# Kernel optimization log

Hardware: AMD Instinct MI355X
Metric: run time of the kernel (lower is better)

## Reference

```python
import jax, jax.numpy as jnp
import numpy as np

B = 2048      # graphs per side
NPG = 40      # nodes per graph
N = B * NPG   # 81920 total nodes
E = 4 * N     # 327680 directed edges
IN_DIM = 74
H = 256
ADD = 8
GCR_LAYERS = 5
MLP1, MLP2 = 1024, 512


def setup_inputs() -> dict:
    key = jax.random.key(0)
    ks = jax.random.split(key, 24)
    n2g = jnp.repeat(jnp.arange(B, dtype=jnp.int32), NPG)
    s = 0.05
    d = {
        'cat_src': jax.random.randint(ks[0], (E,), 0, N, dtype=jnp.int32),
        'cat_dst': jax.random.randint(ks[1], (E,), 0, N, dtype=jnp.int32),
        'cat_n2g': n2g,
        'cat_x': jax.random.normal(ks[2], (N, IN_DIM), jnp.float32),
        'an_src': jax.random.randint(ks[3], (E,), 0, N, dtype=jnp.int32),
        'an_dst': jax.random.randint(ks[4], (E,), 0, N, dtype=jnp.int32),
        'an_n2g': n2g,
        'an_x': jax.random.normal(ks[5], (N, IN_DIM), jnp.float32),
        'add_features': jax.random.normal(ks[6], (B, ADD), jnp.float32),
        # shared GNN params (same module processes cation and anion)
        'W0': jax.random.normal(ks[7], (IN_DIM, H), jnp.float32) * s,
        'b0': jnp.zeros((H,), jnp.float32),
        'gcrW': jax.random.normal(ks[8], (GCR_LAYERS, 2, H, H), jnp.float32) * s,
        'gcrb': jnp.zeros((GCR_LAYERS, 2, H), jnp.float32),
        # MLP head: (2H + ADD) -> 1024 -> 512 -> 1
        'mW1': jax.random.normal(ks[9], (2 * H + ADD, MLP1), jnp.float32) * s,
        'mb1': jnp.zeros((MLP1,), jnp.float32),
        'mW2': jax.random.normal(ks[10], (MLP1, MLP2), jnp.float32) * s,
        'mb2': jnp.zeros((MLP2,), jnp.float32),
        'mW3': jax.random.normal(ks[11], (MLP2, 1), jnp.float32) * s,
        'mb3': jnp.zeros((1,), jnp.float32),
    }
    return d


def _graph_conv(src, dst, x, W, b):
    # DGL GraphConv, norm='both': out = D_in^{-1/2} A^T D_out^{-1/2} x W + b
    ones = jnp.ones(src.shape[0], x.dtype)
    deg_out = jnp.clip(jax.ops.segment_sum(ones, src, num_segments=N), 1.0)
    deg_in = jnp.clip(jax.ops.segment_sum(ones, dst, num_segments=N), 1.0)
    h = x * jax.lax.rsqrt(deg_out)[:, None]
    agg = jax.ops.segment_sum(h[src], dst, num_segments=N)  # [N, d]
    return (agg * jax.lax.rsqrt(deg_in)[:, None]) @ W + b


def _feat_extract(src, dst, n2g, x, W0, b0, gcrW, gcrb):
    h = _graph_conv(src, dst, x, W0, b0)  # no activation after first conv
    for i in range(GCR_LAYERS):
        o1 = _graph_conv(src, dst, h, gcrW[i, 0], gcrb[i, 0])
        o2 = _graph_conv(src, dst, jax.nn.relu(o1), gcrW[i, 1], gcrb[i, 1])
        h = jax.nn.relu(o2)  # res_connection = 0 -> plain replace
    # dgl.sum_nodes readout per graph
    return jax.ops.segment_sum(h, n2g, num_segments=B)  # [B, H]


def _leaky(x):
    return jnp.where(x > 0, x, 0.01 * x)  # nn.LeakyReLU default slope


def reference(cat_src, cat_dst, cat_n2g, cat_x, an_src, an_dst, an_n2g, an_x,
              add_features, W0, b0, gcrW, gcrb, mW1, mb1, mW2, mb2, mW3, mb3):
    cat_feat = _feat_extract(cat_src, cat_dst, cat_n2g, cat_x, W0, b0, gcrW, gcrb)
    an_feat = _feat_extract(an_src, an_dst, an_n2g, an_x, W0, b0, gcrW, gcrb)
    z = jnp.concatenate([cat_feat, an_feat, add_features], axis=1)  # [B, 2H+ADD]
    h = _leaky(z @ mW1 + mb1)
    h = _leaky(h @ mW2 + mb2)
    out = h @ mW3 + mb3  # [B, 1]
    return out.squeeze(-1)
```

## Files before the change

### kernel.cpp

```cpp
#include <hip/hip_runtime.h>


#define NN 81920
#define NN2 163840
#define NE 327680
#define NE2 655360
#define NB 2048
#define NB2 4096
#define H 256
#define INDIM 74
#define KPAD 128
#define ZK 576
#define DEGCAP 32
#define CPITCH 132

typedef unsigned short u16;
typedef __attribute__((ext_vector_type(8))) short short8;
typedef __attribute__((ext_vector_type(4))) float f32x4;

__device__ inline u16 f2b(float f) {
    unsigned u = __builtin_bit_cast(unsigned, f);
    u += 0x7fffu + ((u >> 16) & 1u);
    return (u16)(u >> 16);
}
__device__ inline float b2f(u16 b) {
    unsigned u = ((unsigned)b) << 16;
    return __builtin_bit_cast(float, u);
}
__device__ inline float blo(unsigned u) { return __builtin_bit_cast(float, u << 16); }
__device__ inline float bhi(unsigned u) { return __builtin_bit_cast(float, u & 0xffff0000u); }

__global__ void fill_kernel(const int* __restrict__ cs, const int* __restrict__ cd,
                            const int* __restrict__ as_, const int* __restrict__ ad,
                            int* __restrict__ dego, int* __restrict__ cnti,
                            int* __restrict__ bucket) {
    int e = blockIdx.x * 256 + threadIdx.x;
    if (e < NE2) {
        int s, d;
        if (e < NE) { s = cs[e]; d = cd[e]; }
        else        { s = as_[e - NE] + NN; d = ad[e - NE] + NN; }
        atomicAdd(&dego[s], 1);
        int p = atomicAdd(&cnti[d], 1);
        if (p < DEGCAP) bucket[(size_t)p * NN2 + d] = s;
    }
}

__global__ void rsqrt_kernel(const int* __restrict__ dego, const int* __restrict__ cnti,
                             float* __restrict__ rso, float* __restrict__ rsi) {
    int i = blockIdx.x * 256 + threadIdx.x;
    if (i < NN2) {
        rso[i] = rsqrtf((float)(dego[i] > 1 ? dego[i] : 1));
        rsi[i] = rsqrtf((float)(cnti[i] > 1 ? cnti[i] : 1));
    }
}

__global__ __launch_bounds__(256) void prescale_x_kernel(
        const float* __restrict__ cx, const float* __restrict__ ax,
        const float* __restrict__ rso, u16* __restrict__ xbp) {
    int t = threadIdx.x;
    int node = blockIdx.x * 4 + (t >> 6);
    int lane = t & 63;
    const float* x = (node < NN) ? (cx + (size_t)node * INDIM)
                                 : (ax + (size_t)(node - NN) * INDIM);
    float w = rso[node];
    int f0 = lane * 2, f1 = f0 + 1;
    u16 a = (f0 < INDIM) ? f2b(x[f0] * w) : (u16)0;
    u16 b = (f1 < INDIM) ? f2b(x[f1] * w) : (u16)0;
    ((unsigned*)xbp)[(size_t)node * 64 + lane] = a | ((unsigned)b << 16);
}

__global__ __launch_bounds__(256) void gather_x_kernel(
        const u16* __restrict__ xbp, const int* __restrict__ bucket,
        const int* __restrict__ cnti, const float* __restrict__ rsi,
        u16* __restrict__ out) {
    int node = blockIdx.x * 16 + (threadIdx.x >> 4);
    int fc = (threadIdx.x & 15) * 8;
    int deg = cnti[node]; if (deg > DEGCAP) deg = DEGCAP;
    const int* bk = bucket + node;
    float acc[8] = {};
    for (int base = 0; base < deg; base += 4) {
        int i0 = bk[(size_t)base * NN2];
        int i1 = (base + 1 < deg) ? bk[(size_t)(base + 1) * NN2] : i0;
        int i2 = (base + 2 < deg) ? bk[(size_t)(base + 2) * NN2] : i0;
        int i3 = (base + 3 < deg) ? bk[(size_t)(base + 3) * NN2] : i0;
        float m1 = (base + 1 < deg) ? 1.f : 0.f;
        float m2 = (base + 2 < deg) ? 1.f : 0.f;
        float m3 = (base + 3 < deg) ? 1.f : 0.f;
        uint4 v0 = *(const uint4*)(xbp + (size_t)i0 * KPAD + fc);
        uint4 v1 = *(const uint4*)(xbp + (size_t)i1 * KPAD + fc);
        uint4 v2 = *(const uint4*)(xbp + (size_t)i2 * KPAD + fc);
        uint4 v3 = *(const uint4*)(xbp + (size_t)i3 * KPAD + fc);
        acc[0] += blo(v0.x) + m1 * blo(v1.x) + m2 * blo(v2.x) + m3 * blo(v3.x);
        acc[1] += bhi(v0.x) + m1 * bhi(v1.x) + m2 * bhi(v2.x) + m3 * bhi(v3.x);
        acc[2] += blo(v0.y) + m1 * blo(v1.y) + m2 * blo(v2.y) + m3 * blo(v3.y);
        acc[3] += bhi(v0.y) + m1 * bhi(v1.y) + m2 * bhi(v2.y) + m3 * bhi(v3.y);
        acc[4] += blo(v0.z) + m1 * blo(v1.z) + m2 * blo(v2.z) + m3 * blo(v3.z);
        acc[5] += bhi(v0.z) + m1 * bhi(v1.z) + m2 * bhi(v2.z) + m3 * bhi(v3.z);
        acc[6] += blo(v0.w) + m1 * blo(v1.w) + m2 * blo(v2.w) + m3 * blo(v3.w);
        acc[7] += bhi(v0.w) + m1 * bhi(v1.w) + m2 * bhi(v2.w) + m3 * bhi(v3.w);
    }
    float ri = rsi[node];
    u16 o[8];
#pragma unroll
    for (int i = 0; i < 8; ++i) o[i] = f2b(acc[i] * ri);
    uint4 ov;
    ov.x = o[0] | ((unsigned)o[1] << 16);
    ov.y = o[2] | ((unsigned)o[3] << 16);
    ov.z = o[4] | ((unsigned)o[5] << 16);
    ov.w = o[6] | ((unsigned)o[7] << 16);
    *(uint4*)(out + (size_t)node * KPAD + fc) = ov;
}

__global__ __launch_bounds__(256) void gather_h_kernel(
        const u16* __restrict__ h, const int* __restrict__ bucket,
        const int* __restrict__ cnti, const float* __restrict__ rso,
        const float* __restrict__ rsi, u16* __restrict__ out) {
    int node = blockIdx.x * 8 + (threadIdx.x >> 5);
    int fc = (threadIdx.x & 31) * 8;
    int deg = cnti[node]; if (deg > DEGCAP) deg = DEGCAP;
    const int* bk = bucket + node;
    float acc[8] = {};
    for (int base = 0; base < deg; base += 4) {
        int i0 = bk[(size_t)base * NN2];
        int i1 = (base + 1 < deg) ? bk[(size_t)(base + 1) * NN2] : i0;
        int i2 = (base + 2 < deg) ? bk[(size_t)(base + 2) * NN2] : i0;
        int i3 = (base + 3 < deg) ? bk[(size_t)(base + 3) * NN2] : i0;
        float w0 = rso[i0];
        float w1 = (base + 1 < deg) ? rso[i1] : 0.f;
        float w2 = (base + 2 < deg) ? rso[i2] : 0.f;
        float w3 = (base + 3 < deg) ? rso[i3] : 0.f;
        uint4 v0 = *(const uint4*)(h + (size_t)i0 * H + fc);
        uint4 v1 = *(const uint4*)(h + (size_t)i1 * H + fc);
        uint4 v2 = *(const uint4*)(h + (size_t)i2 * H + fc);
        uint4 v3 = *(const uint4*)(h + (size_t)i3 * H + fc);
        acc[0] += blo(v0.x) * w0 + blo(v1.x) * w1 + blo(v2.x) * w2 + blo(v3.x) * w3;
        acc[1] += bhi(v0.x) * w0 + bhi(v1.x) * w1 + bhi(v2.x) * w2 + bhi(v3.x) * w3;
        acc[2] += blo(v0.y) * w0 + blo(v1.y) * w1 + blo(v2.y) * w2 + blo(v3.y) * w3;
        acc[3] += bhi(v0.y) * w0 + bhi(v1.y) * w1 + bhi(v2.y) * w2 + bhi(v3.y) * w3;
        acc[4] += blo(v0.z) * w0 + blo(v1.z) * w1 + blo(v2.z) * w2 + blo(v3.z) * w3;
        acc[5] += bhi(v0.z) * w0 + bhi(v1.z) * w1 + bhi(v2.z) * w2 + bhi(v3.z) * w3;
        acc[6] += blo(v0.w) * w0 + blo(v1.w) * w1 + blo(v2.w) * w2 + blo(v3.w) * w3;
        acc[7] += bhi(v0.w) * w0 + bhi(v1.w) * w1 + bhi(v2.w) * w2 + bhi(v3.w) * w3;
    }
    float ri = rsi[node];
    u16 o[8];
#pragma unroll
    for (int i = 0; i < 8; ++i) o[i] = f2b(acc[i] * ri);
    uint4 ov;
    ov.x = o[0] | ((unsigned)o[1] << 16);
    ov.y = o[2] | ((unsigned)o[3] << 16);
    ov.z = o[4] | ((unsigned)o[5] << 16);
    ov.w = o[6] | ((unsigned)o[7] << 16);
    *(uint4*)(out + (size_t)node * H + fc) = ov;
}

__global__ void prep_w0_kernel(const float* __restrict__ W0, u16* __restrict__ Wt0) {
    int i = blockIdx.x * 256 + threadIdx.x;
    int n = i >> 7, k = i & 127;
    float v = (k < INDIM) ? W0[(size_t)k * H + n] : 0.f;
    Wt0[i] = f2b(v);
}

__global__ void prep_gcr_kernel(const float* __restrict__ W, u16* __restrict__ Wt) {
    int i = blockIdx.x * 256 + threadIdx.x;
    int l = blockIdx.y;
    int n = i >> 8, k = i & 255;
    Wt[(size_t)l * 65536 + i] = f2b(W[(size_t)l * 65536 + (size_t)k * H + n]);
}

__global__ void prep_w1_kernel(const float* __restrict__ W, u16* __restrict__ Wt) {
    int i = blockIdx.x * 256 + threadIdx.x;
    if (i >= 1024 * ZK) return;
    int n = i / ZK, k = i - n * ZK;
    float v = (k < 520) ? W[(size_t)k * 1024 + n] : 0.f;
    Wt[i] = f2b(v);
}

__global__ void prep_w2_kernel(const float* __restrict__ W, u16* __restrict__ Wt) {
    int i = blockIdx.x * 256 + threadIdx.x;
    int n = i >> 10, k = i & 1023;
    Wt[i] = f2b(W[(size_t)k * 512 + n]);
}

__device__ inline void ldg_lds16(const u16* g, u16* l) {
    __builtin_amdgcn_global_load_lds(
        (const __attribute__((address_space(1))) unsigned int*)g,
        (__attribute__((address_space(3))) unsigned int*)l, 16, 0, 0);
}
__device__ inline float actf(float v, int act) {
    if (act == 1) return fmaxf(v, 0.f);
    if (act == 2) return (v > 0.f) ? v : 0.01f * v;
    return v;
}

__global__ __launch_bounds__(256) void gemm_mfma_kernel(
        const u16* __restrict__ A, int lda,
        const u16* __restrict__ Bt, int ldb,
        const float* __restrict__ bias, u16* __restrict__ C, int ldc,
        int Kiters, int act) {
    __shared__ __align__(16) u16 smem[128 * CPITCH];
    u16* As = smem;
    u16* Bs = smem + 8192;
    int t = threadIdx.x;
    int wave = t >> 6, lane = t & 63;
    int wr = wave >> 1, wc = wave & 1;
    int row0 = blockIdx.y * 128, col0 = blockIdx.x * 128;

    int sr = t >> 3;
    int ksrc = (((t & 7) ^ (sr & 7))) * 8;
    const u16* Ag[4];
    const u16* Bg[4];
#pragma unroll
    for (int c = 0; c < 4; ++c) {
        Ag[c] = A + (size_t)(row0 + c * 32 + sr) * lda + ksrc;
        Bg[c] = Bt + (size_t)(col0 + c * 32 + sr) * ldb + ksrc;
    }
    u16* AsW = As + wave * 512;
    u16* BsW = Bs + wave * 512;

    f32x4 acc[4][4] = {};
    int mrow = lane & 15;
    int q = lane >> 4;

    for (int kt = 0; kt < Kiters; ++kt) {
#pragma unroll
        for (int c = 0; c < 4; ++c) ldg_lds16(Ag[c], AsW + c * 2048);
#pragma unroll
        for (int c = 0; c < 4; ++c) ldg_lds16(Bg[c], BsW + c * 2048);
        __syncthreads();
#pragma unroll
        for (int kk = 0; kk < 2; ++kk) {
            short8 a[4], b[4];
#pragma unroll
            for (int mt = 0; mt < 4; ++mt) {
                int row = wr * 64 + mt * 16 + mrow;
                int seg = (kk * 4 + q) ^ (row & 7);
                a[mt] = *(const short8*)(As + row * 64 + seg * 8);
            }
#pragma unroll
            for (int nt = 0; nt < 4; ++nt) {
                int row = wc * 64 + nt * 16 + mrow;
                int seg = (kk * 4 + q) ^ (row & 7);
                b[nt] = *(const short8*)(Bs + row * 64 + seg * 8);
            }
#pragma unroll
            for (int mt = 0; mt < 4; ++mt)
#pragma unroll
                for (int nt = 0; nt < 4; ++nt)
                    acc[mt][nt] = __builtin_amdgcn_mfma_f32_16x16x32_bf16(
                        a[mt], b[nt], acc[mt][nt], 0, 0, 0);
        }
        __syncthreads();
#pragma unroll
        for (int c = 0; c < 4; ++c) { Ag[c] += 64; Bg[c] += 64; }
    }

#pragma unroll
    for (int mt = 0; mt < 4; ++mt) {
        int rl = wr * 64 + mt * 16 + q * 4;
#pragma unroll
        for (int nt = 0; nt < 4; ++nt) {
            int cl = wc * 64 + nt * 16 + mrow;
            float bv = bias[col0 + cl];
#pragma unroll
            for (int qq = 0; qq < 4; ++qq) {
                float v = actf(acc[mt][nt][qq] + bv, act);
                smem[(size_t)(rl + qq) * CPITCH + cl] = f2b(v);
            }
        }
    }
    __syncthreads();
    int rr = t >> 4;
    int seg = t & 15;
#pragma unroll
    for (int pass = 0; pass < 8; ++pass) {
        int row = pass * 16 + rr;
        uint4 val = *(const uint4*)(smem + (size_t)row * CPITCH + seg * 8);
        *(uint4*)(C + (size_t)(row0 + row) * ldc + col0 + seg * 8) = val;
    }
}

__global__ __launch_bounds__(256) void pool_kernel(const u16* __restrict__ h,
                                                   u16* __restrict__ z) {
    int g = blockIdx.x, f = threadIdx.x;
    float acc = 0.f;
    const u16* base = h + (size_t)g * 40 * H + f;
#pragma unroll
    for (int j = 0; j < 40; ++j) acc += b2f(base[j * H]);
    int zrow = g & (NB - 1);
    int zoff = (g >> 11) * H;
    z[(size_t)zrow * ZK + zoff + f] = f2b(acc);
}

__global__ void copy_add_kernel(const float* __restrict__ add, u16* __restrict__ z) {
    int i = blockIdx.x * 256 + threadIdx.x;
    if (i < NB * 8) {
        int g = i >> 3, a = i & 7;
        z[(size_t)g * ZK + 512 + a] = f2b(add[i]);
    }
}

__global__ void gemv_out_kernel(const u16* __restrict__ A, const float* __restrict__ w,
                                const float* __restrict__ b, float* __restrict__ out, int K) {
    int wave = threadIdx.x >> 6;
    int lane = threadIdx.x & 63;
    int row = blockIdx.x * 4 + wave;
    float acc = 0.f;
    for (int k = lane; k < K; k += 64) acc += b2f(A[(size_t)row * K + k]) * w[k];
#pragma unroll
    for (int off = 32; off > 0; off >>= 1) acc += __shfl_down(acc, off, 64);
    if (lane == 0) out[row] = acc + b[0];
}

extern "C" void kernel_launch(void* const* d_in, const int* in_sizes, int n_in,
                              void* d_out, int out_size, void* d_ws, size_t ws_size,
                              hipStream_t stream) {
    const int*   cat_src = (const int*)d_in[0];
    const int*   cat_dst = (const int*)d_in[1];
    const float* cat_x   = (const float*)d_in[3];
    const int*   an_src  = (const int*)d_in[4];
    const int*   an_dst  = (const int*)d_in[5];
    const float* an_x    = (const float*)d_in[7];
    const float* add_f   = (const float*)d_in[8];
    const float* W0      = (const float*)d_in[9];
    const float* b0      = (const float*)d_in[10];
    const float* gcrW    = (const float*)d_in[11];
    const float* gcrb    = (const float*)d_in[12];
    const float* mW1     = (const float*)d_in[13];
    const float* mb1     = (const float*)d_in[14];
    const float* mW2     = (const float*)d_in[15];
    const float* mb2     = (const float*)d_in[16];
    const float* mW3     = (const float*)d_in[17];
    const float* mb3     = (const float*)d_in[18];
    float* out = (float*)d_out;

    char* p = (char*)d_ws;
    auto alloc = [&](size_t bytes) -> void* {
        void* rp = (void*)p;
        p += (bytes + 255) & ~(size_t)255;
        return rp;
    };
    int*   dego   = (int*)alloc((size_t)NN2 * 4);
    int*   cnti   = (int*)alloc((size_t)NN2 * 4);
    int*   bucket = (int*)alloc((size_t)NN2 * DEGCAP * 4);
    float* rso    = (float*)alloc((size_t)NN2 * 4);
    float* rsi    = (float*)alloc((size_t)NN2 * 4);
    u16*   hA     = (u16*)alloc((size_t)NN2 * H * 2);
    u16*   hB     = (u16*)alloc((size_t)NN2 * H * 2);
    u16*   Wt0    = (u16*)alloc((size_t)H * KPAD * 2);
    u16*   Wtg    = (u16*)alloc((size_t)10 * H * H * 2);
    u16*   Wt1    = (u16*)alloc((size_t)1024 * ZK * 2);
    u16*   Wt2    = (u16*)alloc((size_t)512 * 1024 * 2);
    u16*   zb     = (u16*)alloc((size_t)NB * ZK * 2);
    u16*   m1b    = (u16*)alloc((size_t)NB * 1024 * 2);
    u16*   m2b    = (u16*)alloc((size_t)NB * 512 * 2);
    u16*   xbp    = hA;
    u16*   aggx   = hB;
    (void)ws_size; (void)in_sizes; (void)n_in; (void)out_size;

    prep_w0_kernel<<<(H * KPAD) / 256, 256, 0, stream>>>(W0, Wt0);
    prep_gcr_kernel<<<dim3(H * H / 256, 10), 256, 0, stream>>>(gcrW, Wtg);
    prep_w1_kernel<<<(1024 * ZK + 255) / 256, 256, 0, stream>>>(mW1, Wt1);
    prep_w2_kernel<<<(512 * 1024) / 256, 256, 0, stream>>>(mW2, Wt2);
    hipMemsetAsync(zb, 0, (size_t)NB * ZK * 2, stream);
    hipMemsetAsync(dego, 0, (size_t)NN2 * 4, stream);
    hipMemsetAsync(cnti, 0, (size_t)NN2 * 4, stream);

    fill_kernel<<<NE2 / 256, 256, 0, stream>>>(cat_src, cat_dst, an_src, an_dst,
                                               dego, cnti, bucket);
    rsqrt_kernel<<<NN2 / 256, 256, 0, stream>>>(dego, cnti, rso, rsi);

    prescale_x_kernel<<<NN2 / 4, 256, 0, stream>>>(cat_x, an_x, rso, xbp);
    gather_x_kernel<<<NN2 / 16, 256, 0, stream>>>(xbp, bucket, cnti, rsi, aggx);
    gemm_mfma_kernel<<<dim3(H / 128, NN2 / 128), 256, 0, stream>>>(
        aggx, KPAD, Wt0, KPAD, b0, hA, H, KPAD / 64, 0);

    for (int l = 0; l < 10; ++l) {
        gather_h_kernel<<<NN2 / 8, 256, 0, stream>>>(hA, bucket, cnti, rso, rsi, hB);
        gemm_mfma_kernel<<<dim3(H / 128, NN2 / 128), 256, 0, stream>>>(
            hB, H, Wtg + (size_t)l * H * H, H, gcrb + (size_t)l * H, hA, H,
            H / 64, 1);
    }
    pool_kernel<<<NB2, 256, 0, stream>>>(hA, zb);
    copy_add_kernel<<<(NB * 8 + 255) / 256, 256, 0, stream>>>(add_f, zb);

    gemm_mfma_kernel<<<dim3(1024 / 128, NB / 128), 256, 0, stream>>>(
        zb, ZK, Wt1, ZK, mb1, m1b, 1024, ZK / 64, 2);
    gemm_mfma_kernel<<<dim3(512 / 128, NB / 128), 256, 0, stream>>>(
        m1b, 1024, Wt2, 1024, mb2, m2b, 512, 1024 / 64, 2);
    gemv_out_kernel<<<NB / 4, 256, 0, stream>>>(m2b, mW3, mb3, out, 512);
}
```

Measured before the change: 1.489 ms.

## Replace capped strided bucket adjacency with exact CSR built by prefix scan

Replaces the column-strided, degree-capped bucket array with a proper CSR built from a count pass, a three-stage prefix scan, and an atomic scatter. Gather kernels now read each node's neighbour list from contiguous memory instead of reading one element per stride of NN2. This also removes the DEGCAP truncation, so nodes with more in-edges than the cap are no longer silently dropped. The cost is four extra small kernel launches plus a second pass over the edges in setup, and the neighbour order within a row is nondeterministic because it comes from atomics.

Result: no change. 1.504 ms (+1.0%).

```diff
diff --git a/kernel.cpp b/kernel.cpp
--- a/kernel.cpp
+++ b/kernel.cpp
@@ -11,8 +11,8 @@
 #define INDIM 74
 #define KPAD 128
 #define ZK 576
-#define DEGCAP 32
 #define CPITCH 132
+#define SCANB 160
 
 typedef unsigned short u16;
 typedef __attribute__((ext_vector_type(8))) short short8;
@@ -30,18 +30,66 @@
 __device__ inline float blo(unsigned u) { return __builtin_bit_cast(float, u << 16); }
 __device__ inline float bhi(unsigned u) { return __builtin_bit_cast(float, u & 0xffff0000u); }
 
-__global__ void fill_kernel(const int* __restrict__ cs, const int* __restrict__ cd,
-                            const int* __restrict__ as_, const int* __restrict__ ad,
-                            int* __restrict__ dego, int* __restrict__ cnti,
-                            int* __restrict__ bucket) {
+__global__ void count_kernel(const int* __restrict__ cs, const int* __restrict__ cd,
+                             const int* __restrict__ as_, const int* __restrict__ ad,
+                             int* __restrict__ dego, int* __restrict__ cnti) {
     int e = blockIdx.x * 256 + threadIdx.x;
     if (e < NE2) {
         int s, d;
         if (e < NE) { s = cs[e]; d = cd[e]; }
         else        { s = as_[e - NE] + NN; d = ad[e - NE] + NN; }
         atomicAdd(&dego[s], 1);
-        int p = atomicAdd(&cnti[d], 1);
-        if (p < DEGCAP) bucket[(size_t)p * NN2 + d] = s;
+        atomicAdd(&cnti[d], 1);
+    }
+}
+
+__global__ __launch_bounds__(1024) void scan1_kernel(const int* __restrict__ cnti,
+                                                     int* __restrict__ rpe,
+                                                     int* __restrict__ bsum) {
+    __shared__ int buf[1024];
+    int b = blockIdx.x, t = threadIdx.x;
+    int i = b * 1024 + t;
+    int v = cnti[i];
+    buf[t] = v;
+    __syncthreads();
+    for (int off = 1; off < 1024; off <<= 1) {
+        int x = (t >= off) ? buf[t - off] : 0;
+        __syncthreads();
+        buf[t] += x;
+        __syncthreads();
+    }
+    rpe[i] = buf[t] - v;
+    if (t == 1023) bsum[b] = buf[t];
+}
+
+__global__ void scan2_kernel(const int* __restrict__ bsum, int* __restrict__ bscan) {
+    if (threadIdx.x == 0) {
+        int acc = 0;
+        for (int i = 0; i < SCANB; ++i) { bscan[i] = acc; acc += bsum[i]; }
+        bscan[SCANB] = acc;
+    }
+}
+
+__global__ __launch_bounds__(1024) void scan3_kernel(const int* __restrict__ rpe,
+                                                     const int* __restrict__ bscan,
+                                                     int* __restrict__ rp) {
+    int b = blockIdx.x, t = threadIdx.x;
+    int i = b * 1024 + t;
+    rp[i] = rpe[i] + bscan[b];
+    if (i == NN2 - 1) rp[NN2] = bscan[SCANB];
+}
+
+__global__ void scatter_kernel(const int* __restrict__ cs, const int* __restrict__ cd,
+                               const int* __restrict__ as_, const int* __restrict__ ad,
+                               const int* __restrict__ rp, int* __restrict__ cursor,
+                               int* __restrict__ csr) {
+    int e = blockIdx.x * 256 + threadIdx.x;
+    if (e < NE2) {
+        int s, d;
+        if (e < NE) { s = cs[e]; d = cd[e]; }
+        else        { s = as_[e - NE] + NN; d = ad[e - NE] + NN; }
+        int p = atomicAdd(&cursor[d], 1);
+        csr[rp[d] + p] = s;
     }
 }
 
@@ -70,19 +118,20 @@
 }
 
 __global__ __launch_bounds__(256) void gather_x_kernel(
-        const u16* __restrict__ xbp, const int* __restrict__ bucket,
-        const int* __restrict__ cnti, const float* __restrict__ rsi,
+        const u16* __restrict__ xbp, const int* __restrict__ rp,
+        const int* __restrict__ csr, const float* __restrict__ rsi,
         u16* __restrict__ out) {
     int node = blockIdx.x * 16 + (threadIdx.x >> 4);
     int fc = (threadIdx.x & 15) * 8;
-    int deg = cnti[node]; if (deg > DEGCAP) deg = DEGCAP;
-    const int* bk = bucket + node;
+    int s0 = rp[node];
+    int deg = rp[node + 1] - s0;
+    const int* bk = csr + s0;
     float acc[8] = {};
     for (int base = 0; base < deg; base += 4) {
-        int i0 = bk[(size_t)base * NN2];
-        int i1 = (base + 1 < deg) ? bk[(size_t)(base + 1) * NN2] : i0;
-        int i2 = (base + 2 < deg) ? bk[(size_t)(base + 2) * NN2] : i0;
-        int i3 = (base + 3 < deg) ? bk[(size_t)(base + 3) * NN2] : i0;
+        int i0 = bk[base];
+        int i1 = (base + 1 < deg) ? bk[base + 1] : i0;
+        int i2 = (base + 2 < deg) ? bk[base + 2] : i0;
+        int i3 = (base + 3 < deg) ? bk[base + 3] : i0;
         float m1 = (base + 1 < deg) ? 1.f : 0.f;
         float m2 = (base + 2 < deg) ? 1.f : 0.f;
         float m3 = (base + 3 < deg) ? 1.f : 0.f;
@@ -112,19 +161,20 @@
 }
 
 __global__ __launch_bounds__(256) void gather_h_kernel(
-        const u16* __restrict__ h, const int* __restrict__ bucket,
-        const int* __restrict__ cnti, const float* __restrict__ rso,
+        const u16* __restrict__ h, const int* __restrict__ rp,
+        const int* __restrict__ csr, const float* __restrict__ rso,
         const float* __restrict__ rsi, u16* __restrict__ out) {
     int node = blockIdx.x * 8 + (threadIdx.x >> 5);
     int fc = (threadIdx.x & 31) * 8;
-    int deg = cnti[node]; if (deg > DEGCAP) deg = DEGCAP;
-    const int* bk = bucket + node;
+    int s0 = rp[node];
+    int deg = rp[node + 1] - s0;
+    const int* bk = csr + s0;
     float acc[8] = {};
     for (int base = 0; base < deg; base += 4) {
-        int i0 = bk[(size_t)base * NN2];
-        int i1 = (base + 1 < deg) ? bk[(size_t)(base + 1) * NN2] : i0;
-        int i2 = (base + 2 < deg) ? bk[(size_t)(base + 2) * NN2] : i0;
-        int i3 = (base + 3 < deg) ? bk[(size_t)(base + 3) * NN2] : i0;
+        int i0 = bk[base];
+        int i1 = (base + 1 < deg) ? bk[base + 1] : i0;
+        int i2 = (base + 2 < deg) ? bk[base + 2] : i0;
+        int i3 = (base + 3 < deg) ? bk[base + 3] : i0;
         float w0 = rso[i0];
         float w1 = (base + 1 < deg) ? rso[i1] : 0.f;
         float w2 = (base + 2 < deg) ? rso[i2] : 0.f;
@@ -336,13 +386,18 @@
 
     char* p = (char*)d_ws;
     auto alloc = [&](size_t bytes) -> void* {
-        void* rp = (void*)p;
+        void* rp_ = (void*)p;
         p += (bytes + 255) & ~(size_t)255;
-        return rp;
+        return rp_;
     };
     int*   dego   = (int*)alloc((size_t)NN2 * 4);
     int*   cnti   = (int*)alloc((size_t)NN2 * 4);
-    int*   bucket = (int*)alloc((size_t)NN2 * DEGCAP * 4);
+    int*   rp     = (int*)alloc((size_t)(NN2 + 1) * 4);
+    int*   rpe    = (int*)alloc((size_t)NN2 * 4);
+    int*   cursor = (int*)alloc((size_t)NN2 * 4);
+    int*   csr    = (int*)alloc((size_t)NE2 * 4);
+    int*   bsum   = (int*)alloc((size_t)SCANB * 4);
+    int*   bscan  = (int*)alloc((size_t)(SCANB + 1) * 4);
     float* rso    = (float*)alloc((size_t)NN2 * 4);
     float* rsi    = (float*)alloc((size_t)NN2 * 4);
     u16*   hA     = (u16*)alloc((size_t)NN2 * H * 2);
@@ -365,18 +420,24 @@
     hipMemsetAsync(zb, 0, (size_t)NB * ZK * 2, stream);
     hipMemsetAsync(dego, 0, (size_t)NN2 * 4, stream);
     hipMemsetAsync(cnti, 0, (size_t)NN2 * 4, stream);
-
-    fill_kernel<<<NE2 / 256, 256, 0, stream>>>(cat_src, cat_dst, an_src, an_dst,
-                                               dego, cnti, bucket);
+    hipMemsetAsync(cursor, 0, (size_t)NN2 * 4, stream);
+
+    count_kernel<<<NE2 / 256, 256, 0, stream>>>(cat_src, cat_dst, an_src, an_dst,
+                                                dego, cnti);
     rsqrt_kernel<<<NN2 / 256, 256, 0, stream>>>(dego, cnti, rso, rsi);
+    scan1_kernel<<<SCANB, 1024, 0, stream>>>(cnti, rpe, bsum);
+    scan2_kernel<<<1, 64, 0, stream>>>(bsum, bscan);
+    scan3_kernel<<<SCANB, 1024, 0, stream>>>(rpe, bscan, rp);
+    scatter_kernel<<<NE2 / 256, 256, 0, stream>>>(cat_src, cat_dst, an_src, an_dst,
+                                                  rp, cursor, csr);
 
     prescale_x_kernel<<<NN2 / 4, 256, 0, stream>>>(cat_x, an_x, rso, xbp);
-    gather_x_kernel<<<NN2 / 16, 256, 0, stream>>>(xbp, bucket, cnti, rsi, aggx);
+    gather_x_kernel<<<NN2 / 16, 256, 0, stream>>>(xbp, rp, csr, rsi, aggx);
     gemm_mfma_kernel<<<dim3(H / 128, NN2 / 128), 256, 0, stream>>>(
         aggx, KPAD, Wt0, KPAD, b0, hA, H, KPAD / 64, 0);
 
     for (int l = 0; l < 10; ++l) {
-        gather_h_kernel<<<NN2 / 8, 256, 0, stream>>>(hA, bucket, cnti, rso, rsi, hB);
+        gather_h_kernel<<<NN2 / 8, 256, 0, stream>>>(hA, rp, csr, rso, rsi, hB);
         gemm_mfma_kernel<<<dim3(H / 128, NN2 / 128), 256, 0, stream>>>(
             hB, H, Wtg + (size_t)l * H * H, H, gcrb + (size_t)l * H, hA, H,
             H / 64, 1);
```
